# Kernel optimization log

Measured on AMD Instinct MI355X. Metric: run time of the kernel, lower is better.

Reference implementation:

```python
import jax, jax.numpy as jnp
import numpy as np

DIM = 768
H = 12          # num query heads
KV = 6          # num kv heads
GS = H // KV    # group size = 2
HD = DIM // H   # head dim = 64


def setup_inputs() -> dict:
    key = jax.random.key(0)
    ks = jax.random.split(key, 6)
    B, P = 8, 1024
    s = DIM ** -0.5
    x = jax.random.normal(ks[0], (B, P, DIM), dtype=jnp.float32)
    Wq = jax.random.normal(ks[1], (DIM, DIM), dtype=jnp.float32) * s
    Wk = jax.random.normal(ks[2], (DIM, KV * HD), dtype=jnp.float32) * s
    Wv = jax.random.normal(ks[3], (DIM, KV * HD), dtype=jnp.float32) * s
    Wp = jax.random.normal(ks[4], (DIM, DIM), dtype=jnp.float32) * s
    bp = jnp.zeros((DIM,), dtype=jnp.float32)
    return {"x": x, "Wq": Wq, "Wk": Wk, "Wv": Wv, "Wp": Wp, "bp": bp}


def reference(x, Wq, Wk, Wv, Wp, bp):
    B, P, C = x.shape
    scale = HD ** -0.5
    # projections; consecutive heads i*GS..(i+1)*GS-1 form kv-group i (torch.split dim=1)
    q = (x @ Wq).reshape(B, P, KV, GS, HD).transpose(0, 2, 3, 1, 4) * scale  # [B,KV,GS,P,d]
    k = (x @ Wk).reshape(B, P, KV, HD).transpose(0, 2, 1, 3)                 # [B,KV,P,d]
    v = (x @ Wv).reshape(B, P, KV, HD).transpose(0, 2, 1, 3)                 # [B,KV,P,d]

    scores = jnp.einsum('bghqd,bgkd->bghqk', q, k)      # [B,KV,GS,P,P]
    w = jax.nn.softmax(scores, axis=-1)                  # attn_drop=0 (eval)
    att = jnp.einsum('bghqk,bgkd->bghqd', w, v)          # [B,KV,GS,P,d]

    # per-group row-matched gaussian-ish noise (torch get_gaussian), vectorized over KV groups
    y = P * HD
    flat = att.reshape(B, KV, GS, y)                     # rows = groups within kv-group
    M = jax.random.uniform(jax.random.key(42), (KV, GS, y), dtype=flat.dtype)
    di = jnp.arange(min(GS, y))
    M = M.at[:, di, di].set(0.0)                         # sparse: zero diagonal
    m_mean = M.mean(axis=-1, keepdims=True)
    m_std = jnp.std(M, axis=-1, ddof=1, keepdims=True)   # torch.std is unbiased
    m_std = jnp.where(m_std == 0, jnp.ones_like(m_std), m_std)
    Z = (M - m_mean) / m_std                             # [KV,GS,y], shared across batch
    r_mean = flat.mean(axis=-1, keepdims=True)           # [B,KV,GS,1]
    r_std = jnp.std(flat, axis=-1, ddof=1, keepdims=True)
    flat = flat - (Z[None] * r_std + r_mean)

    att = flat.reshape(B, KV, GS, P, HD).reshape(B, H, P, HD)
    out = att.transpose(0, 2, 1, 3).reshape(B, P, C) @ Wp + bp  # proj_drop=0
    return out
```

## Files before the change

kernel.cpp:

```cpp
#include <hip/hip_runtime.h>
#include <hip/hip_bf16.h>
#include <math.h>


#define NTHREADS 256

typedef __bf16 bf16x8 __attribute__((ext_vector_type(8)));
typedef float f32x4 __attribute__((ext_vector_type(4)));

#define MFMA16(a, b, c) __builtin_amdgcn_mfma_f32_16x16x32_bf16(a, b, c, 0, 0, 0)

#define QSCALE 0.18033688011112042f

__device__ __forceinline__ float fexp2(float x) {
#if __has_builtin(__builtin_amdgcn_exp2f)
    return __builtin_amdgcn_exp2f(x);
#else
    return __expf(x * 0.6931471805599453f);
#endif
}

__device__ __forceinline__ void gload16(const void* g, void* l) {
    __builtin_amdgcn_global_load_lds(
        (const __attribute__((address_space(1))) void*)g,
        (__attribute__((address_space(3))) void*)l, 16, 0, 0);
}

__device__ __forceinline__ unsigned rotl_u32(unsigned x, int r) {
    return (x << r) | (x >> (32 - r));
}
__device__ __forceinline__ void threefry_0_42(unsigned x0, unsigned x1,
                                              unsigned& o0, unsigned& o1) {
    const unsigned ks0 = 0u, ks1 = 42u, ks2 = 0u ^ 42u ^ 0x1BD11BDAu;
    x0 += ks0; x1 += ks1;
#define R4(a,b,c,d) \
    x0 += x1; x1 = rotl_u32(x1,a); x1 ^= x0; \
    x0 += x1; x1 = rotl_u32(x1,b); x1 ^= x0; \
    x0 += x1; x1 = rotl_u32(x1,c); x1 ^= x0; \
    x0 += x1; x1 = rotl_u32(x1,d); x1 ^= x0;
    R4(13,15,26,6)   x0 += ks1; x1 += ks2 + 1u;
    R4(17,29,16,24)  x0 += ks2; x1 += ks0 + 2u;
    R4(13,15,26,6)   x0 += ks0; x1 += ks1 + 3u;
    R4(17,29,16,24)  x0 += ks1; x1 += ks2 + 4u;
    R4(13,15,26,6)   x0 += ks2; x1 += ks0 + 5u;
#undef R4
    o0 = x0; o1 = x1;
}
__device__ __forceinline__ float tf_uniform(unsigned i) {
    unsigned o0, o1;
    threefry_0_42(0u, i, o0, o1);
    unsigned bits = o0 ^ o1;
    return __uint_as_float((bits >> 9) | 0x3f800000u) - 1.0f;
}

__device__ __forceinline__ float wave_sum64(float v) {
#pragma unroll
    for (int off = 32; off; off >>= 1) v += __shfl_xor(v, off, 64);
    return v;
}

__device__ __forceinline__ unsigned short bf16_rne(float x) {
    unsigned u = __float_as_uint(x);
    return (unsigned short)((u + 0x7fffu + ((u >> 16) & 1u)) >> 16);
}
__device__ __forceinline__ unsigned pack_bf16x2(float lo, float hi) {
    unsigned ul = __float_as_uint(lo), uh = __float_as_uint(hi);
    unsigned rl = ul + 0x7fffu + ((ul >> 16) & 1u);
    unsigned rh = uh + 0x7fffu + ((uh >> 16) & 1u);
    return __builtin_amdgcn_perm(rh, rl, 0x07060302u);
}
__device__ __forceinline__ float bfu(unsigned v) {
    return __uint_as_float(v << 16);
}


__global__ __launch_bounds__(NTHREADS) void prep_k(
    const float* __restrict__ x, const float* __restrict__ Wq,
    const float* __restrict__ Wk, const float* __restrict__ Wv,
    const float* __restrict__ Wp,
    unsigned short* __restrict__ xb, unsigned short* __restrict__ wstk,
    unsigned short* __restrict__ wpt,
    unsigned short* __restrict__ zb, float* __restrict__ zpart)
{
    __shared__ float rbuf[8];
    int blk = blockIdx.x;
    if (blk < 1536) {
#pragma unroll
        for (int j = 0; j < 4; ++j) {
            int i = blk * 1024 + j * 256 + threadIdx.x;
            float4 v = ((const float4*)x)[i];
            uint2 u;
            u.x = pack_bf16x2(v.x, v.y);
            u.y = pack_bf16x2(v.z, v.w);
            int f0 = i * 4;
            int row = f0 / 768, col = f0 - row * 768;
            int kc = col >> 6, kin = col & 63;
            int kh = kin >> 5, g = (kin >> 3) & 3, e = col & 7;
            int chunk = row >> 4, cl = row & 15;
            size_t a = (((size_t)(kc * 512 + chunk)) * 2 + kh) * 512
                       + (g * 16 + cl) * 8 + e;
            *(uint2*)&xb[a] = u;
        }
    } else if (blk < 1920) {
        int zc = blk - 1536;
        int row = zc >> 5, chunk = zc & 31;
        int g = row & 1;
        int j0 = chunk * 2048;
        float sum = 0.f, sumsq = 0.f;
        for (int t = threadIdx.x; t < 2048; t += NTHREADS) {
            int j = j0 + t;
            unsigned i = (unsigned)row * 65536u + (unsigned)j;
            float m = tf_uniform(i);
            if (j == g) m = 0.f;
            zb[i] = bf16_rne(m);
            sum += m; sumsq += m * m;
        }
        sum = wave_sum64(sum); sumsq = wave_sum64(sumsq);
        int lane = threadIdx.x & 63, wv = threadIdx.x >> 6;
        if (lane == 0) { rbuf[wv] = sum; rbuf[4 + wv] = sumsq; }
        __syncthreads();
        if (threadIdx.x == 0) {
            zpart[zc * 2]     = rbuf[0] + rbuf[1] + rbuf[2] + rbuf[3];
            zpart[zc * 2 + 1] = rbuf[4] + rbuf[5] + rbuf[6] + rbuf[7];
        }
    } else {
        int id = blk - 1920;
        const float* W; unsigned short* dstbuf; int N, rowbase, NC;
        if (id < 144)      { W = Wq; dstbuf = wstk; N = 768; rowbase = 0;    NC = 96; }
        else if (id < 216) { W = Wk; dstbuf = wstk; N = 384; rowbase = 768;  NC = 96; id -= 144; }
        else if (id < 288) { W = Wv; dstbuf = wstk; N = 384; rowbase = 1152; NC = 96; id -= 216; }
        else               { W = Wp; dstbuf = wpt;  N = 768; rowbase = 0;    NC = 48; id -= 288; }
        int ntn = N >> 6;
        int kt = id / ntn, nt = id % ntn;
        int k0 = kt * 64, n0 = nt * 64;
        int t = threadIdx.x;
        int tn = t & 63, tk = t >> 6;
        float r[16];
#pragma unroll
        for (int j = 0; j < 16; ++j)
            r[j] = W[(size_t)(k0 + tk * 16 + j) * N + n0 + tn];
        uint4 u0, u1;
        u0.x = pack_bf16x2(r[0], r[1]);   u0.y = pack_bf16x2(r[2], r[3]);
        u0.z = pack_bf16x2(r[4], r[5]);   u0.w = pack_bf16x2(r[6], r[7]);
        u1.x = pack_bf16x2(r[8], r[9]);   u1.y = pack_bf16x2(r[10], r[11]);
        u1.z = pack_bf16x2(r[12], r[13]); u1.w = pack_bf16x2(r[14], r[15]);
        int rowg = rowbase + n0 + tn;
        int chunk = rowg >> 4, cl = rowg & 15;
        int kc = k0 >> 6;
        int kh = tk >> 1, g0 = (tk & 1) * 2;
        size_t base = (((size_t)(kc * NC + chunk)) * 2 + kh) * 512 + cl * 8;
        *(uint4*)&dstbuf[base + g0 * 128]       = u0;
        *(uint4*)&dstbuf[base + (g0 + 1) * 128] = u1;
    }
}

__device__ __forceinline__ void mfma_tile128x256(
    const unsigned short* __restrict__ Afb, int nca,
    const unsigned short* __restrict__ Bfb,
    int row0, int col0,
    unsigned short* As, unsigned short* Bs, f32x4 acc[4][4])
{
    const int tid = threadIdx.x;
    const int lane = tid & 63, w = tid >> 6;
    const int c = lane & 15, g = lane >> 4;
    const int wm = w & 1, wn = w >> 1;

#pragma unroll
    for (int mi = 0; mi < 4; ++mi)
#pragma unroll
        for (int ni = 0; ni < 4; ++ni) acc[mi][ni] = (f32x4){0.f, 0.f, 0.f, 0.f};

    const unsigned short* Abase = Afb + (size_t)(row0 >> 4) * 1024;
    const unsigned short* Bbase = Bfb + (size_t)(col0 >> 4) * 1024;

    for (int kc = 0; kc < 12; ++kc) {
        const unsigned short* a = Abase + (size_t)kc * nca * 1024;
        const unsigned short* bb = Bbase + (size_t)kc * 512 * 1024;
        __syncthreads();
        gload16(a  + tid * 8,         As + tid * 8);
        gload16(a  + tid * 8 + 4096,  As + tid * 8 + 4096);
        gload16(bb + tid * 8,         Bs + tid * 8);
        gload16(bb + tid * 8 + 4096,  Bs + tid * 8 + 4096);
        gload16(bb + tid * 8 + 8192,  Bs + tid * 8 + 8192);
        gload16(bb + tid * 8 + 12288, Bs + tid * 8 + 12288);
        __syncthreads();
#pragma unroll
        for (int ks = 0; ks < 2; ++ks) {
            bf16x8 aA[4], bB[4];
#pragma unroll
            for (int mi = 0; mi < 4; ++mi)
                aA[mi] = *(const bf16x8*)&As[(wm * 4 + mi) * 1024 + ks * 512 + g * 128 + c * 8];
#pragma unroll
            for (int ni = 0; ni < 4; ++ni)
                bB[ni] = *(const bf16x8*)&Bs[(wn * 4 + ni) * 1024 + ks * 512 + g * 128 + c * 8];
#pragma unroll
            for (int mi = 0; mi < 4; ++mi)
#pragma unroll
                for (int ni = 0; ni < 4; ++ni)
                    acc[mi][ni] = MFMA16(aA[mi], bB[ni], acc[mi][ni]);
        }
    }
}

__global__ __launch_bounds__(512) void qkv_mfma_k(
    const unsigned short* __restrict__ xb, const unsigned short* __restrict__ wstk,
    unsigned short* __restrict__ qbh, unsigned short* __restrict__ kb2,
    unsigned short* __restrict__ vb2)
{
    __shared__ unsigned short As[8192];
    __shared__ unsigned short Bs[16384];
    int id = blockIdx.x;
    int xcd = id & 7, slot = id >> 3;
    int col0i = xcd + ((slot & 3) << 3);
    int row0i = slot >> 2;
    int row0 = row0i * 128, col0 = col0i * 256;
    f32x4 acc[4][4];
    mfma_tile128x256(wstk, 96, xb, row0, col0, As, Bs, acc);

    const int tid = threadIdx.x;
    const int w = tid >> 6, lane = tid & 63;
    const int c = lane & 15, g = lane >> 4;
    const int wm = w & 1, wn = w >> 1;

#pragma unroll
    for (int mi = 0; mi < 4; ++mi) {
        int ocb = row0 + wm * 64 + mi * 16;
        int ocol = ocb + g * 4;
#pragma unroll
        for (int ni = 0; ni < 4; ++ni) {
            int pglob = col0 + wn * 64 + ni * 16 + c;
            int b = pglob >> 10, pin = pglob & 1023;
            if (ocb < 768) {
                ushort4 u;
                u.x = bf16_rne(acc[mi][ni][0] * QSCALE);
                u.y = bf16_rne(acc[mi][ni][1] * QSCALE);
                u.z = bf16_rne(acc[mi][ni][2] * QSCALE);
                u.w = bf16_rne(acc[mi][ni][3] * QSCALE);
                int h = ocol >> 6, d0 = ocol & 63;
                *(ushort4*)&qbh[(((size_t)b * 12 + h) * 1024 + pin) * 64 + d0] = u;
            } else if (ocb < 1152) {
                int kcol = ocol - 768;
                int kv = kcol >> 6, d0 = kcol & 63;
                int kt = pin >> 7, key = pin & 127;
                ushort4 u;
                u.x = bf16_rne(acc[mi][ni][0]);
                u.y = bf16_rne(acc[mi][ni][1]);
                u.z = bf16_rne(acc[mi][ni][2]);
                u.w = bf16_rne(acc[mi][ni][3]);
                *(ushort4*)&kb2[((((size_t)(b * 6 + kv) * 8 + kt) * 8 + (d0 >> 3)) * 128
                                 + key) * 8 + (d0 & 7)] = u;
            } else {
                int kt = pin >> 7, pg = (pin & 127) >> 3, p8 = pin & 7;
#pragma unroll
                for (int r = 0; r < 4; ++r) {
                    int vcol = ocol + r - 1152;
                    int kv = vcol >> 6, d = vcol & 63;
                    vb2[((((size_t)(b * 6 + kv) * 8 + kt) * 16 + pg) * 64 + d) * 8 + p8]
                        = bf16_rne(acc[mi][ni][r]);
                }
            }
        }
    }
}

__global__ __launch_bounds__(512) void proj_mfma_k(
    const unsigned short* __restrict__ attb, const unsigned short* __restrict__ wpt,
    const float* __restrict__ bp, float* __restrict__ out)
{
    __shared__ unsigned short As[8192];
    __shared__ unsigned short Bs[16384];
    int id = blockIdx.x;
    int xcd = id & 7, slot = id >> 3;
    int col0i = xcd + ((slot & 3) << 3);
    int row0i = slot >> 2;
    int row0 = row0i * 128, col0 = col0i * 256;
    f32x4 acc[4][4];
    mfma_tile128x256(wpt, 48, attb, row0, col0, As, Bs, acc);

    const int tid = threadIdx.x;
    const int w = tid >> 6, lane = tid & 63;
    const int c = lane & 15, g = lane >> 4;
    const int wm = w & 1, wn = w >> 1;
#pragma unroll
    for (int mi = 0; mi < 4; ++mi) {
        int ocol = row0 + wm * 64 + mi * 16 + g * 4;
        float4 bias = *(const float4*)&bp[ocol];
#pragma unroll
        for (int ni = 0; ni < 4; ++ni) {
            int p = col0 + wn * 64 + ni * 16 + c;
            float4 u;
            u.x = acc[mi][ni][0] + bias.x;
            u.y = acc[mi][ni][1] + bias.y;
            u.z = acc[mi][ni][2] + bias.z;
            u.w = acc[mi][ni][3] + bias.w;
            *(float4*)&out[(size_t)p * 768 + ocol] = u;
        }
    }
}

#define LDP 140
__global__ __launch_bounds__(NTHREADS) void attn_mfma_k(
    const unsigned short* __restrict__ qbh, const unsigned short* __restrict__ kb2,
    const unsigned short* __restrict__ vb2, unsigned short* __restrict__ attb,
    float* __restrict__ spart)
{
    __shared__ unsigned short P_lds[4 * 32 * LDP];
    __shared__ float l_s[4][32];
    __shared__ float sbuf[8];

    int id = blockIdx.x;
    int xcd = id & 7, slot = id >> 3;
    int grp = slot % 6, member = slot / 6;
    int g48 = xcd + 8 * grp;
    int b = g48 / 6, kv = g48 % 6;
    int h = kv * 2 + (member & 1);
    int qtile = member >> 1;
    const int qt0 = qtile * 128;

    const int tid = threadIdx.x;
    const int w = tid >> 6, lane = tid & 63;
    const int c = lane & 15, g = lane >> 4;

    const unsigned short* qh = qbh + (((size_t)b * 12 + h) * 1024 + qt0 + w * 32) * 64;
    const unsigned short* kbase = kb2 + ((size_t)(b * 6 + kv) * 8) * 8192;
    const unsigned short* vbase = vb2 + ((size_t)(b * 6 + kv) * 8) * 8192;
    unsigned short* Pw = P_lds + w * 32 * LDP;

    bf16x8 bQ[2][2];
#pragma unroll
    for (int ks = 0; ks < 2; ++ks) {
        bQ[ks][0] = *(const bf16x8*)(qh + (size_t)(c) * 64 + ks * 32 + g * 8);
        bQ[ks][1] = *(const bf16x8*)(qh + (size_t)(16 + c) * 64 + ks * 32 + g * 8);
    }

    f32x4 O[2][4];
#pragma unroll
    for (int i = 0; i < 2; ++i)
#pragma unroll
        for (int j = 0; j < 4; ++j) O[i][j] = (f32x4){0.f, 0.f, 0.f, 0.f};
    float l_r[2] = {0.f, 0.f};

    for (int t = 0; t < 8; ++t) {
        const unsigned short* kt = kbase + (size_t)t * 8192;
        const unsigned short* vt = vbase + (size_t)t * 8192;

        bf16x8 aK[2][8];
#pragma unroll
        for (int ks = 0; ks < 2; ++ks)
#pragma unroll
            for (int mb = 0; mb < 8; ++mb)
                aK[ks][mb] = *(const bf16x8*)(kt + ((size_t)(ks * 4 + g) * 128 + mb * 16 + c) * 8);

        f32x4 S[8][2];
#pragma unroll
        for (int mb = 0; mb < 8; ++mb) {
            S[mb][0] = (f32x4){0.f, 0.f, 0.f, 0.f};
            S[mb][1] = (f32x4){0.f, 0.f, 0.f, 0.f};
        }
#pragma unroll
        for (int ks = 0; ks < 2; ++ks)
#pragma unroll
            for (int mb = 0; mb < 8; ++mb) {
                S[mb][0] = MFMA16(aK[ks][mb], bQ[ks][0], S[mb][0]);
                S[mb][1] = MFMA16(aK[ks][mb], bQ[ks][1], S[mb][1]);
            }

        bf16x8 bV[4][4];
#pragma unroll
        for (int ks = 0; ks < 4; ++ks)
#pragma unroll
            for (int nb = 0; nb < 4; ++nb)
                bV[ks][nb] = *(const bf16x8*)(vt + ((size_t)(ks * 4 + g) * 64 + nb * 16 + c) * 8);

#pragma unroll
        for (int qn = 0; qn < 2; ++qn) {
            float lt = 0.f;
#pragma unroll
            for (int mb = 0; mb < 8; ++mb) {
                float p0 = fexp2(S[mb][qn][0]);
                float p1 = fexp2(S[mb][qn][1]);
                float p2 = fexp2(S[mb][qn][2]);
                float p3 = fexp2(S[mb][qn][3]);
                lt += (p0 + p1) + (p2 + p3);
                uint2 uu;
                uu.x = pack_bf16x2(p0, p1);
                uu.y = pack_bf16x2(p2, p3);
                *(uint2*)&Pw[(size_t)(qn * 16 + c) * LDP + mb * 16 + g * 4] = uu;
            }
            lt += __shfl_xor(lt, 16, 64);
            lt += __shfl_xor(lt, 32, 64);
            l_r[qn] += lt;
        }

#pragma unroll
        for (int ks = 0; ks < 4; ++ks) {
            bf16x8 aP0 = *(const bf16x8*)&Pw[(size_t)(c) * LDP + ks * 32 + g * 8];
            bf16x8 aP1 = *(const bf16x8*)&Pw[(size_t)(16 + c) * LDP + ks * 32 + g * 8];
#pragma unroll
            for (int nb = 0; nb < 4; ++nb) {
                O[0][nb] = MFMA16(aP0, bV[ks][nb], O[0][nb]);
                O[1][nb] = MFMA16(aP1, bV[ks][nb], O[1][nb]);
            }
        }
    }
    if (g == 0) { l_s[w][c] = l_r[0]; l_s[w][16 + c] = l_r[1]; }
    f32x4 li0 = *(f32x4*)&l_s[w][g * 4];
    f32x4 li1 = *(f32x4*)&l_s[w][16 + g * 4];
    float inv0[4], inv1[4];
#pragma unroll
    for (int r = 0; r < 4; ++r) { inv0[r] = 1.f / li0[r]; inv1[r] = 1.f / li1[r]; }
    int rowblk = (b * 1024 + qt0 + w * 32) >> 4;
    float psum = 0.f, psumsq = 0.f;
#pragma unroll
    for (int r = 0; r < 4; ++r) {
        int cl = g * 4 + r;
#pragma unroll
        for (int nb = 0; nb < 4; ++nb) {
            float o0 = O[0][nb][r] * inv0[r];
            float o1 = O[1][nb][r] * inv1[r];
            psum += o0 + o1;
            psumsq += o0 * o0 + o1 * o1;
            int kh = nb >> 1, gb = (nb & 1) * 2 + (c >> 3), e = c & 7;
            size_t a0 = (((size_t)h * 512 + rowblk) * 2 + kh) * 512
                        + (gb * 16 + cl) * 8 + e;
            size_t a1 = (((size_t)h * 512 + rowblk + 1) * 2 + kh) * 512
                        + (gb * 16 + cl) * 8 + e;
            attb[a0] = bf16_rne(o0);
            attb[a1] = bf16_rne(o1);
        }
    }
    psum = wave_sum64(psum); psumsq = wave_sum64(psumsq);
    if (lane == 0) { sbuf[w] = psum; sbuf[4 + w] = psumsq; }
    __syncthreads();
    if (tid == 0) {
        int idx = ((b * 12 + h) * 8 + qtile) * 2;
        spart[idx]     = sbuf[0] + sbuf[1] + sbuf[2] + sbuf[3];
        spart[idx + 1] = sbuf[4] + sbuf[5] + sbuf[6] + sbuf[7];
    }
}

__global__ __launch_bounds__(NTHREADS) void stats2_k(
    unsigned short* __restrict__ attb, const unsigned short* __restrict__ zb,
    const float* __restrict__ spart, const float* __restrict__ zpart)
{
    int blk = blockIdx.x;
    int bh = blk >> 3, ch = blk & 7;
    int b = bh / 12, h = bh % 12;
    float zs = 0.f, zs2 = 0.f, rs = 0.f, rs2 = 0.f;
#pragma unroll
    for (int cc = 0; cc < 32; ++cc) {
        zs  += zpart[(h * 32 + cc) * 2];
        zs2 += zpart[(h * 32 + cc) * 2 + 1];
    }
#pragma unroll
    for (int cc = 0; cc < 8; ++cc) {
        rs  += spart[(bh * 8 + cc) * 2];
        rs2 += spart[(bh * 8 + cc) * 2 + 1];
    }
    float m_mean = zs * (1.f / 65536.f);
    float m_var  = (zs2 - 65536.f * m_mean * m_mean) * (1.f / 65535.f);
    float m_sd   = sqrtf(fmaxf(m_var, 0.f));
    if (m_sd == 0.f) m_sd = 1.f;
    float r_mean = rs * (1.f / 65536.f);
    float r_var  = (rs2 - 65536.f * r_mean * r_mean) * (1.f / 65535.f);
    float r_sd   = sqrtf(fmaxf(r_var, 0.f));
    float a = r_sd / m_sd;
    float bc = m_mean * a - r_mean;

    const unsigned short* zrow = zb + (size_t)h * 65536 + (size_t)ch * 8192;
    for (int f = threadIdx.x; f < 1024; f += NTHREADS) {
        int p = f >> 3, dq = (f & 7) * 8;
        int row = b * 1024 + ch * 128 + p;
        int chunk = row >> 4, cl = row & 15;
        int kh = dq >> 5, gb = (dq >> 3) & 3;
        size_t aoff = (((size_t)h * 512 + chunk) * 2 + kh) * 512 + (gb * 16 + cl) * 8;
        unsigned short* ptr = attb + aoff;
        uint4 u = *(const uint4*)ptr;
        uint4 zu = *(const uint4*)(zrow + (size_t)f * 8);
        float v0 = bfu(u.x)       - bfu(zu.x)       * a + bc;
        float v1 = bfu(u.x >> 16) - bfu(zu.x >> 16) * a + bc;
        float v2 = bfu(u.y)       - bfu(zu.y)       * a + bc;
        float v3 = bfu(u.y >> 16) - bfu(zu.y >> 16) * a + bc;
        float v4 = bfu(u.z)       - bfu(zu.z)       * a + bc;
        float v5 = bfu(u.z >> 16) - bfu(zu.z >> 16) * a + bc;
        float v6 = bfu(u.w)       - bfu(zu.w)       * a + bc;
        float v7 = bfu(u.w >> 16) - bfu(zu.w >> 16) * a + bc;
        uint4 o;
        o.x = pack_bf16x2(v0, v1);
        o.y = pack_bf16x2(v2, v3);
        o.z = pack_bf16x2(v4, v5);
        o.w = pack_bf16x2(v6, v7);
        *(uint4*)ptr = o;
    }
}

extern "C" void kernel_launch(void* const* d_in, const int* in_sizes, int n_in,
                              void* d_out, int out_size, void* d_ws, size_t ws_size,
                              hipStream_t stream) {
    const float* x  = (const float*)d_in[0];
    const float* Wq = (const float*)d_in[1];
    const float* Wk = (const float*)d_in[2];
    const float* Wv = (const float*)d_in[3];
    const float* Wp = (const float*)d_in[4];
    const float* bp = (const float*)d_in[5];
    float* out = (float*)d_out;

    float* ws    = (float*)d_ws;
    float* zpart = ws;
    float* spart = zpart + 768;
    unsigned short* zb   = (unsigned short*)(spart + 1536);
    unsigned short* xb   = zb + 786432;
    unsigned short* wstk = xb + 6291456;
    unsigned short* wpt  = wstk + 1179648;
    unsigned short* qbh  = wpt + 589824;
    unsigned short* kb2  = qbh + 6291456;
    unsigned short* vb2  = kb2 + 3145728;
    unsigned short* attb = vb2 + 3145728;

    prep_k<<<2352, NTHREADS, 0, stream>>>(x, Wq, Wk, Wv, Wp,
                                          xb, wstk, wpt, zb, zpart);
    qkv_mfma_k<<<384, 512, 0, stream>>>(xb, wstk, qbh, kb2, vb2);
    attn_mfma_k<<<768, NTHREADS, 0, stream>>>(qbh, kb2, vb2, attb, spart);
    stats2_k<<<768, NTHREADS, 0, stream>>>(attb, zb, spart, zpart);
    proj_mfma_k<<<192, 512, 0, stream>>>(attb, wpt, bp, out);
}
```

Measured before the change: 188.4 us.

## Halve attention query tile to 16 rows per wave, doubling grid size

The attention kernel now processes 64 query rows per block (16 per wave) instead of 128, and the grid doubles to 1536 blocks. This cuts per-wave register and LDS use, which raises occupancy and spreads the work over more blocks. In exchange, each K/V tile is loaded from global/L2 twice as often overall, and each K fragment is reused by half as many MFMAs. The partial-statistics buffer and the stats kernel's reduction loop are resized to 16 chunks, and the workspace offsets are shifted to match.

New measurement: 211.9 us. 12.5% more time.

```diff
diff --git a/kernel.cpp b/kernel.cpp
--- a/kernel.cpp
+++ b/kernel.cpp
@@ -304,8 +304,8 @@
     const unsigned short* __restrict__ vb2, unsigned short* __restrict__ attb,
     float* __restrict__ spart)
 {
-    __shared__ unsigned short P_lds[4 * 32 * LDP];
-    __shared__ float l_s[4][32];
+    __shared__ unsigned short P_lds[4 * 16 * LDP];
+    __shared__ float l_s[4][16];
     __shared__ float sbuf[8];
 
     int id = blockIdx.x;
@@ -314,31 +314,27 @@
     int g48 = xcd + 8 * grp;
     int b = g48 / 6, kv = g48 % 6;
     int h = kv * 2 + (member & 1);
-    int qtile = member >> 1;
-    const int qt0 = qtile * 128;
+    int qt64 = member >> 1;
+    const int qt0 = qt64 * 64;
 
     const int tid = threadIdx.x;
     const int w = tid >> 6, lane = tid & 63;
     const int c = lane & 15, g = lane >> 4;
 
-    const unsigned short* qh = qbh + (((size_t)b * 12 + h) * 1024 + qt0 + w * 32) * 64;
+    const unsigned short* qh = qbh + (((size_t)b * 12 + h) * 1024 + qt0 + w * 16) * 64;
     const unsigned short* kbase = kb2 + ((size_t)(b * 6 + kv) * 8) * 8192;
     const unsigned short* vbase = vb2 + ((size_t)(b * 6 + kv) * 8) * 8192;
-    unsigned short* Pw = P_lds + w * 32 * LDP;
-
-    bf16x8 bQ[2][2];
-#pragma unroll
-    for (int ks = 0; ks < 2; ++ks) {
-        bQ[ks][0] = *(const bf16x8*)(qh + (size_t)(c) * 64 + ks * 32 + g * 8);
-        bQ[ks][1] = *(const bf16x8*)(qh + (size_t)(16 + c) * 64 + ks * 32 + g * 8);
-    }
-
-    f32x4 O[2][4];
-#pragma unroll
-    for (int i = 0; i < 2; ++i)
-#pragma unroll
-        for (int j = 0; j < 4; ++j) O[i][j] = (f32x4){0.f, 0.f, 0.f, 0.f};
-    float l_r[2] = {0.f, 0.f};
+    unsigned short* Pw = P_lds + w * 16 * LDP;
+
+    bf16x8 bQ[2];
+#pragma unroll
+    for (int ks = 0; ks < 2; ++ks)
+        bQ[ks] = *(const bf16x8*)(qh + (size_t)(c) * 64 + ks * 32 + g * 8);
+
+    f32x4 O[4];
+#pragma unroll
+    for (int j = 0; j < 4; ++j) O[j] = (f32x4){0.f, 0.f, 0.f, 0.f};
+    float l_r = 0.f;
 
     for (int t = 0; t < 8; ++t) {
         const unsigned short* kt = kbase + (size_t)t * 8192;
@@ -351,19 +347,14 @@
             for (int mb = 0; mb < 8; ++mb)
                 aK[ks][mb] = *(const bf16x8*)(kt + ((size_t)(ks * 4 + g) * 128 + mb * 16 + c) * 8);
 
-        f32x4 S[8][2];
-#pragma unroll
-        for (int mb = 0; mb < 8; ++mb) {
-            S[mb][0] = (f32x4){0.f, 0.f, 0.f, 0.f};
-            S[mb][1] = (f32x4){0.f, 0.f, 0.f, 0.f};
-        }
+        f32x4 S[8];
+#pragma unroll
+        for (int mb = 0; mb < 8; ++mb) S[mb] = (f32x4){0.f, 0.f, 0.f, 0.f};
 #pragma unroll
         for (int ks = 0; ks < 2; ++ks)
 #pragma unroll
-            for (int mb = 0; mb < 8; ++mb) {
-                S[mb][0] = MFMA16(aK[ks][mb], bQ[ks][0], S[mb][0]);
-                S[mb][1] = MFMA16(aK[ks][mb], bQ[ks][1], S[mb][1]);
-            }
+            for (int mb = 0; mb < 8; ++mb)
+                S[mb] = MFMA16(aK[ks][mb], bQ[ks], S[mb]);
 
         bf16x8 bV[4][4];
 #pragma unroll
@@ -372,68 +363,57 @@
             for (int nb = 0; nb < 4; ++nb)
                 bV[ks][nb] = *(const bf16x8*)(vt + ((size_t)(ks * 4 + g) * 64 + nb * 16 + c) * 8);
 
-#pragma unroll
-        for (int qn = 0; qn < 2; ++qn) {
-            float lt = 0.f;
-#pragma unroll
-            for (int mb = 0; mb < 8; ++mb) {
-                float p0 = fexp2(S[mb][qn][0]);
-                float p1 = fexp2(S[mb][qn][1]);
-                float p2 = fexp2(S[mb][qn][2]);
-                float p3 = fexp2(S[mb][qn][3]);
-                lt += (p0 + p1) + (p2 + p3);
-                uint2 uu;
-                uu.x = pack_bf16x2(p0, p1);
-                uu.y = pack_bf16x2(p2, p3);
-                *(uint2*)&Pw[(size_t)(qn * 16 + c) * LDP + mb * 16 + g * 4] = uu;
-            }
-            lt += __shfl_xor(lt, 16, 64);
-            lt += __shfl_xor(lt, 32, 64);
-            l_r[qn] += lt;
-        }
+        float lt = 0.f;
+#pragma unroll
+        for (int mb = 0; mb < 8; ++mb) {
+            float p0 = fexp2(S[mb][0]);
+            float p1 = fexp2(S[mb][1]);
+            float p2 = fexp2(S[mb][2]);
+            float p3 = fexp2(S[mb][3]);
+            lt += (p0 + p1) + (p2 + p3);
+            uint2 uu;
+            uu.x = pack_bf16x2(p0, p1);
+            uu.y = pack_bf16x2(p2, p3);
+            *(uint2*)&Pw[(size_t)c * LDP + mb * 16 + g * 4] = uu;
+        }
+        lt += __shfl_xor(lt, 16, 64);
+        lt += __shfl_xor(lt, 32, 64);
+        l_r += lt;
 
 #pragma unroll
         for (int ks = 0; ks < 4; ++ks) {
-            bf16x8 aP0 = *(const bf16x8*)&Pw[(size_t)(c) * LDP + ks * 32 + g * 8];
-            bf16x8 aP1 = *(const bf16x8*)&Pw[(size_t)(16 + c) * LDP + ks * 32 + g * 8];
-#pragma unroll
-            for (int nb = 0; nb < 4; ++nb) {
-                O[0][nb] = MFMA16(aP0, bV[ks][nb], O[0][nb]);
-                O[1][nb] = MFMA16(aP1, bV[ks][nb], O[1][nb]);
-            }
-        }
-    }
-    if (g == 0) { l_s[w][c] = l_r[0]; l_s[w][16 + c] = l_r[1]; }
-    f32x4 li0 = *(f32x4*)&l_s[w][g * 4];
-    f32x4 li1 = *(f32x4*)&l_s[w][16 + g * 4];
-    float inv0[4], inv1[4];
-#pragma unroll
-    for (int r = 0; r < 4; ++r) { inv0[r] = 1.f / li0[r]; inv1[r] = 1.f / li1[r]; }
-    int rowblk = (b * 1024 + qt0 + w * 32) >> 4;
+            bf16x8 aP = *(const bf16x8*)&Pw[(size_t)c * LDP + ks * 32 + g * 8];
+#pragma unroll
+            for (int nb = 0; nb < 4; ++nb)
+                O[nb] = MFMA16(aP, bV[ks][nb], O[nb]);
+        }
+    }
+    if (g == 0) l_s[w][c] = l_r;
+    f32x4 li = *(f32x4*)&l_s[w][g * 4];
+    float inv[4];
+#pragma unroll
+    for (int r = 0; r < 4; ++r) inv[r] = 1.f / li[r];
+    int rowblk = (b * 1024 + qt0 + w * 16) >> 4;
     float psum = 0.f, psumsq = 0.f;
 #pragma unroll
     for (int r = 0; r < 4; ++r) {
         int cl = g * 4 + r;
 #pragma unroll
         for (int nb = 0; nb < 4; ++nb) {
-            float o0 = O[0][nb][r] * inv0[r];
-            float o1 = O[1][nb][r] * inv1[r];
-            psum += o0 + o1;
-            psumsq += o0 * o0 + o1 * o1;
+            float o0 = O[nb][r] * inv[r];
+            psum += o0;
+            psumsq += o0 * o0;
             int kh = nb >> 1, gb = (nb & 1) * 2 + (c >> 3), e = c & 7;
             size_t a0 = (((size_t)h * 512 + rowblk) * 2 + kh) * 512
                         + (gb * 16 + cl) * 8 + e;
-            size_t a1 = (((size_t)h * 512 + rowblk + 1) * 2 + kh) * 512
-                        + (gb * 16 + cl) * 8 + e;
             attb[a0] = bf16_rne(o0);
-            attb[a1] = bf16_rne(o1);
         }
     }
     psum = wave_sum64(psum); psumsq = wave_sum64(psumsq);
     if (lane == 0) { sbuf[w] = psum; sbuf[4 + w] = psumsq; }
     __syncthreads();
     if (tid == 0) {
-        int idx = ((b * 12 + h) * 8 + qtile) * 2;
+        int idx = ((b * 12 + h) * 16 + qt64) * 2;
         spart[idx]     = sbuf[0] + sbuf[1] + sbuf[2] + sbuf[3];
         spart[idx + 1] = sbuf[4] + sbuf[5] + sbuf[6] + sbuf[7];
     }
@@ -453,9 +433,9 @@
         zs2 += zpart[(h * 32 + cc) * 2 + 1];
     }
 #pragma unroll
-    for (int cc = 0; cc < 8; ++cc) {
-        rs  += spart[(bh * 8 + cc) * 2];
-        rs2 += spart[(bh * 8 + cc) * 2 + 1];
+    for (int cc = 0; cc < 16; ++cc) {
+        rs  += spart[(bh * 16 + cc) * 2];
+        rs2 += spart[(bh * 16 + cc) * 2 + 1];
     }
     float m_mean = zs * (1.f / 65536.f);
     float m_var  = (zs2 - 65536.f * m_mean * m_mean) * (1.f / 65535.f);
@@ -508,7 +488,7 @@
     float* ws    = (float*)d_ws;
     float* zpart = ws;
     float* spart = zpart + 768;
-    unsigned short* zb   = (unsigned short*)(spart + 1536);
+    unsigned short* zb   = (unsigned short*)(spart + 3072);
     unsigned short* xb   = zb + 786432;
     unsigned short* wstk = xb + 6291456;
     unsigned short* wpt  = wstk + 1179648;
@@ -520,7 +500,7 @@
     prep_k<<<2352, NTHREADS, 0, stream>>>(x, Wq, Wk, Wv, Wp,
                                           xb, wstk, wpt, zb, zpart);
     qkv_mfma_k<<<384, 512, 0, stream>>>(xb, wstk, qbh, kb2, vb2);
-    attn_mfma_k<<<768, NTHREADS, 0, stream>>>(qbh, kb2, vb2, attb, spart);
+    attn_mfma_k<<<1536, NTHREADS, 0, stream>>>(qbh, kb2, vb2, attb, spart);
     stats2_k<<<768, NTHREADS, 0, stream>>>(attb, zb, spart, zpart);
     proj_mfma_k<<<192, 512, 0, stream>>>(attb, wpt, bp, out);
 }
```

## Stage K/V tiles in shared memory and halve the P buffer per wave

Applied to the files above, without the earlier changes.

Each block now cooperatively copies the K and V tiles for each key step into LDS with direct global-to-LDS loads, bracketed by barriers. Before, each of the four waves loaded the same tiles from global memory into registers on its own. The P-times-V product is now split per query half, so each wave's P scratch holds 16 rows instead of 32 and the register-resident K and V fragments go away. This cuts redundant global traffic and register pressure, but adds two block barriers per step with no double buffering and more LDS reads.

Measured after the change: 218.9 us. 1.16x slower.

```diff
diff --git a/kernel.cpp b/kernel.cpp
--- a/kernel.cpp
+++ b/kernel.cpp
@@ -304,7 +304,9 @@
     const unsigned short* __restrict__ vb2, unsigned short* __restrict__ attb,
     float* __restrict__ spart)
 {
-    __shared__ unsigned short P_lds[4 * 32 * LDP];
+    __shared__ unsigned short Ks[8192];
+    __shared__ unsigned short Vs[8192];
+    __shared__ unsigned short P_lds[4 * 16 * LDP];
     __shared__ float l_s[4][32];
     __shared__ float sbuf[8];
 
@@ -324,7 +326,7 @@
     const unsigned short* qh = qbh + (((size_t)b * 12 + h) * 1024 + qt0 + w * 32) * 64;
     const unsigned short* kbase = kb2 + ((size_t)(b * 6 + kv) * 8) * 8192;
     const unsigned short* vbase = vb2 + ((size_t)(b * 6 + kv) * 8) * 8192;
-    unsigned short* Pw = P_lds + w * 32 * LDP;
+    unsigned short* Pw = P_lds + w * 16 * LDP;
 
     bf16x8 bQ[2][2];
 #pragma unroll
@@ -344,12 +346,16 @@
         const unsigned short* kt = kbase + (size_t)t * 8192;
         const unsigned short* vt = vbase + (size_t)t * 8192;
 
-        bf16x8 aK[2][8];
-#pragma unroll
-        for (int ks = 0; ks < 2; ++ks)
-#pragma unroll
-            for (int mb = 0; mb < 8; ++mb)
-                aK[ks][mb] = *(const bf16x8*)(kt + ((size_t)(ks * 4 + g) * 128 + mb * 16 + c) * 8);
+        __syncthreads();
+        gload16(kt + tid * 8,        Ks + tid * 8);
+        gload16(kt + tid * 8 + 2048, Ks + tid * 8 + 2048);
+        gload16(kt + tid * 8 + 4096, Ks + tid * 8 + 4096);
+        gload16(kt + tid * 8 + 6144, Ks + tid * 8 + 6144);
+        gload16(vt + tid * 8,        Vs + tid * 8);
+        gload16(vt + tid * 8 + 2048, Vs + tid * 8 + 2048);
+        gload16(vt + tid * 8 + 4096, Vs + tid * 8 + 4096);
+        gload16(vt + tid * 8 + 6144, Vs + tid * 8 + 6144);
+        __syncthreads();
 
         f32x4 S[8][2];
 #pragma unroll
@@ -361,16 +367,10 @@
         for (int ks = 0; ks < 2; ++ks)
 #pragma unroll
             for (int mb = 0; mb < 8; ++mb) {
-                S[mb][0] = MFMA16(aK[ks][mb], bQ[ks][0], S[mb][0]);
-                S[mb][1] = MFMA16(aK[ks][mb], bQ[ks][1], S[mb][1]);
+                bf16x8 aK = *(const bf16x8*)&Ks[((ks * 4 + g) * 128 + mb * 16 + c) * 8];
+                S[mb][0] = MFMA16(aK, bQ[ks][0], S[mb][0]);
+                S[mb][1] = MFMA16(aK, bQ[ks][1], S[mb][1]);
             }
-
-        bf16x8 bV[4][4];
-#pragma unroll
-        for (int ks = 0; ks < 4; ++ks)
-#pragma unroll
-            for (int nb = 0; nb < 4; ++nb)
-                bV[ks][nb] = *(const bf16x8*)(vt + ((size_t)(ks * 4 + g) * 64 + nb * 16 + c) * 8);
 
 #pragma unroll
         for (int qn = 0; qn < 2; ++qn) {
@@ -385,21 +385,19 @@
                 uint2 uu;
                 uu.x = pack_bf16x2(p0, p1);
                 uu.y = pack_bf16x2(p2, p3);
-                *(uint2*)&Pw[(size_t)(qn * 16 + c) * LDP + mb * 16 + g * 4] = uu;
+                *(uint2*)&Pw[(size_t)c * LDP + mb * 16 + g * 4] = uu;
             }
             lt += __shfl_xor(lt, 16, 64);
             lt += __shfl_xor(lt, 32, 64);
             l_r[qn] += lt;
-        }
-
-#pragma unroll
-        for (int ks = 0; ks < 4; ++ks) {
-            bf16x8 aP0 = *(const bf16x8*)&Pw[(size_t)(c) * LDP + ks * 32 + g * 8];
-            bf16x8 aP1 = *(const bf16x8*)&Pw[(size_t)(16 + c) * LDP + ks * 32 + g * 8];
-#pragma unroll
-            for (int nb = 0; nb < 4; ++nb) {
-                O[0][nb] = MFMA16(aP0, bV[ks][nb], O[0][nb]);
-                O[1][nb] = MFMA16(aP1, bV[ks][nb], O[1][nb]);
+#pragma unroll
+            for (int ks = 0; ks < 4; ++ks) {
+                bf16x8 aP = *(const bf16x8*)&Pw[(size_t)c * LDP + ks * 32 + g * 8];
+#pragma unroll
+                for (int nb = 0; nb < 4; ++nb) {
+                    bf16x8 bV = *(const bf16x8*)&Vs[((ks * 4 + g) * 64 + nb * 16 + c) * 8];
+                    O[qn][nb] = MFMA16(aP, bV, O[qn][nb]);
+                }
             }
         }
     }
```
